# Optimization experiments

Measured on AMD Instinct MI355X. Metric: run time of the kernel, lower is better.

The kernel has to match this reference:

```python
import jax, jax.numpy as jnp
import numpy as np

EPS = 1e-5
H_PN = 64      # PointNet hidden
D = 768        # hidden_dim
SEM = 512


def _ln(x, g, b):
    m = jnp.mean(x, axis=-1, keepdims=True)
    v = jnp.var(x, axis=-1, keepdims=True)
    return (x - m) * jax.lax.rsqrt(v + EPS) * g + b


def _pointnet(x, idx, num_nodes, w1, b1, g1, be1, w2, b2, w3, b3, g2, be2, w4, b4):
    # mlp1: Linear -> LN -> ReLU -> Linear  on [P, 3] points
    h = jax.nn.relu(_ln(x @ w1 + b1, g1, be1)) @ w2 + b2          # [P, 64]
    # scatter_max into per-node features (torch_scatter fills empty segments with 0)
    xg = jax.ops.segment_max(h, idx, num_segments=num_nodes)       # [num_nodes, 64]
    xg = jnp.where(jnp.isfinite(xg), xg, 0.0)
    # mlp2: Linear -> LN -> ReLU -> Linear
    return jax.nn.relu(_ln(xg @ w3 + b3, g2, be2)) @ w4 + b4       # [num_nodes, D]


def setup_inputs() -> dict:
    key = jax.random.key(0)
    ks = jax.random.split(key, 40)
    P = 1048576
    NN = 16384
    d = {
        "x_pos": jax.random.normal(ks[0], (P, 3), jnp.float32),
        "pos_batch_idx": jax.random.randint(ks[1], (P,), 0, NN),
        "x_aff": jax.random.normal(ks[2], (P, 3), jnp.float32),
        "aff_batch_idx": jax.random.randint(ks[3], (P,), 0, NN),
        "x_sem": jax.random.normal(ks[4], (NN, SEM), jnp.float32),
        "num_nodes": NN,
    }
    def lin(k, fan_in, fan_out):
        k1, k2 = jax.random.split(k)
        return (jax.random.normal(k1, (fan_in, fan_out), jnp.float32) * 0.02,
                jax.random.normal(k2, (fan_out,), jnp.float32) * 0.02)
    i = 5
    for pfx in ("pos", "aff"):
        d[pfx + "_w1"], d[pfx + "_b1"] = lin(ks[i], 3, H_PN); i += 1
        d[pfx + "_g1"] = jnp.ones((H_PN,), jnp.float32)
        d[pfx + "_be1"] = jnp.zeros((H_PN,), jnp.float32)
        d[pfx + "_w2"], d[pfx + "_b2"] = lin(ks[i], H_PN, H_PN); i += 1
        d[pfx + "_w3"], d[pfx + "_b3"] = lin(ks[i], H_PN, D); i += 1
        d[pfx + "_g2"] = jnp.ones((D,), jnp.float32)
        d[pfx + "_be2"] = jnp.zeros((D,), jnp.float32)
        d[pfx + "_w4"], d[pfx + "_b4"] = lin(ks[i], D, D); i += 1
    d["sem_w"], d["sem_b"] = lin(ks[i], SEM, D); i += 1
    d["fus_w"], d["fus_b"] = lin(ks[i], 3 * D, D); i += 1
    d["fus_g"] = jnp.ones((D,), jnp.float32)
    d["fus_be"] = jnp.zeros((D,), jnp.float32)
    return d


def reference(x_pos, pos_batch_idx, x_aff, aff_batch_idx, x_sem, num_nodes,
              pos_w1, pos_b1, pos_g1, pos_be1, pos_w2, pos_b2, pos_w3, pos_b3,
              pos_g2, pos_be2, pos_w4, pos_b4,
              aff_w1, aff_b1, aff_g1, aff_be1, aff_w2, aff_b2, aff_w3, aff_b3,
              aff_g2, aff_be2, aff_w4, aff_b4,
              sem_w, sem_b, fus_w, fus_b, fus_g, fus_be):
    h_pos = _pointnet(x_pos, pos_batch_idx, num_nodes, pos_w1, pos_b1, pos_g1,
                      pos_be1, pos_w2, pos_b2, pos_w3, pos_b3, pos_g2, pos_be2,
                      pos_w4, pos_b4)
    h_aff = _pointnet(x_aff, aff_batch_idx, num_nodes, aff_w1, aff_b1, aff_g1,
                      aff_be1, aff_w2, aff_b2, aff_w3, aff_b3, aff_g2, aff_be2,
                      aff_w4, aff_b4)
    h_sem = x_sem @ sem_w + sem_b                                  # [NN, D]
    h = jnp.concatenate([h_pos, h_aff, h_sem], axis=-1)            # [NN, 3D]
    return jax.nn.relu(_ln(h @ fus_w + fus_b, fus_g, fus_be))      # [NN, D]
```

## Files before the change

### kernel.cpp

```cpp
#include <hip/hip_runtime.h>

typedef __attribute__((ext_vector_type(8))) __bf16 bf16x8;
typedef __attribute__((ext_vector_type(4))) float floatx4;

#define NN 16384
#define EPS 1e-5f

__device__ __forceinline__ unsigned short f2b(float f) {
  unsigned u = __float_as_uint(f);
  u += 0x7fffu + ((u >> 16) & 1u);
  return (unsigned short)(u >> 16);
}
__device__ __forceinline__ float b2f(unsigned short u) {
  return __uint_as_float(((unsigned)u) << 16);
}

__device__ __forceinline__ void gl_lds16(const void* g, void* l) {
  __builtin_amdgcn_global_load_lds(
      (const __attribute__((address_space(1))) void*)(unsigned long long)g,
      (__attribute__((address_space(3))) void*)(unsigned long long)l, 16, 0, 0);
}

__global__ void RoboNodeEncoder_88424786690347_kernel() {}

__global__ __launch_bounds__(256) void zero_u32(unsigned* __restrict__ p, int n) {
  int i = blockIdx.x * blockDim.x + threadIdx.x;
  if (i < n) p[i] = 0u;
}

__global__ __launch_bounds__(256) void convert3(const float* __restrict__ a, int na,
                                                const float* __restrict__ b, int nb,
                                                const float* __restrict__ c, int nc,
                                                unsigned short* __restrict__ out) {
  int i = blockIdx.x * 256 + threadIdx.x;
  int total = na + nb + nc;
  if (i >= total) return;
  float v;
  if (i < na) v = a[i];
  else if (i < na + nb) v = b[i - na];
  else v = c[i - na - nb];
  out[i] = f2b(v);
}

__global__ __launch_bounds__(256) void convert_sem(const float* __restrict__ in,
                                                   unsigned short* __restrict__ out) {
  int i = blockIdx.x * 256 + threadIdx.x;
  const float4* p = reinterpret_cast<const float4*>(in);
  float4 fa = p[2 * i];
  float4 fb = p[2 * i + 1];
  uint4 pk;
  pk.x = (unsigned)f2b(fa.x) | ((unsigned)f2b(fa.y) << 16);
  pk.y = (unsigned)f2b(fa.z) | ((unsigned)f2b(fa.w) << 16);
  pk.z = (unsigned)f2b(fb.x) | ((unsigned)f2b(fb.y) << 16);
  pk.w = (unsigned)f2b(fb.z) | ((unsigned)f2b(fb.w) << 16);
  reinterpret_cast<uint4*>(out)[i] = pk;
}

__global__ __launch_bounds__(256) void transpose_f32_b16(const float* __restrict__ in,
                                                         unsigned short* __restrict__ out,
                                                         int R, int C) {
  __shared__ float t[32][33];
  int bx = blockIdx.x * 32, by = blockIdx.y * 32;
  int x = threadIdx.x, y = threadIdx.y;
#pragma unroll
  for (int i = 0; i < 32; i += 8) t[y + i][x] = in[(size_t)(by + y + i) * C + bx + x];
  __syncthreads();
#pragma unroll
  for (int i = 0; i < 32; i += 8) out[(size_t)(bx + y + i) * R + by + x] = f2b(t[x][y + i]);
}

__global__ __launch_bounds__(256) void transpose_w3_pair(const float* __restrict__ pw3,
                                                         const float* __restrict__ aw3,
                                                         unsigned short* __restrict__ w3T) {
  __shared__ float t[32][33];
  const float* in = blockIdx.z ? aw3 : pw3;
  unsigned short* out = w3T + (size_t)blockIdx.z * 768 * 64;
  int R = 64, C = 768;
  int bx = blockIdx.x * 32, by = blockIdx.y * 32;
  int x = threadIdx.x, y = threadIdx.y;
#pragma unroll
  for (int i = 0; i < 32; i += 8) t[y + i][x] = in[(size_t)(by + y + i) * C + bx + x];
  __syncthreads();
#pragma unroll
  for (int i = 0; i < 32; i += 8) out[(size_t)(bx + y + i) * R + by + x] = f2b(t[x][y + i]);
}

__global__ void prep_pointnet2(const float* __restrict__ w1p, const float* __restrict__ b1p,
                               const float* __restrict__ g1p,
                               const float* __restrict__ w1a, const float* __restrict__ b1a,
                               const float* __restrict__ g1a,
                               const float* __restrict__ w2p, const float* __restrict__ w2a,
                               float* __restrict__ G2, float* __restrict__ Mq2,
                               unsigned short* __restrict__ w2T) {
  int br = blockIdx.x;
  const float* w1 = br ? w1a : w1p;
  const float* b1 = br ? b1a : b1p;
  const float* g1 = br ? g1a : g1p;
  const float* w2 = br ? w2a : w2p;
  float* G = G2 + br * 256;
  float* Mq = Mq2 + br * 16;
  unsigned short* w2t = w2T + br * 4096;
  int k = threadIdx.x;
#pragma unroll
  for (int n = 0; n < 64; n++) w2t[n * 64 + k] = f2b(w2[k * 64 + n]);
  float c[4] = {w1[k], w1[64 + k], w1[128 + k], b1[k]};
#pragma unroll
  for (int a = 0; a < 4; a++) {
    float s = c[a];
#pragma unroll
    for (int off = 32; off > 0; off >>= 1) s += __shfl_xor(s, off, 64);
    c[a] -= s * (1.f / 64.f);
  }
  float g = g1[k];
#pragma unroll
  for (int a = 0; a < 4; a++) G[a * 64 + k] = c[a] * g;
  const int AA[10] = {0, 1, 2, 3, 0, 0, 0, 1, 1, 2};
  const int BB[10] = {0, 1, 2, 3, 1, 2, 3, 2, 3, 3};
#pragma unroll
  for (int t = 0; t < 10; t++) {
    float s = c[AA[t]] * c[BB[t]];
#pragma unroll
    for (int off = 32; off > 0; off >>= 1) s += __shfl_xor(s, off, 64);
    s *= (1.f / 64.f);
    if (t >= 4) s *= 2.f;
    if (k == 0) Mq[t] = s;
  }
}

__global__ __launch_bounds__(256) void hist_bucket(const int* __restrict__ pos_idx,
                                                   const int* __restrict__ aff_idx, int P,
                                                   unsigned* __restrict__ cntB) {
  __shared__ unsigned lc[512];
  int br = blockIdx.y;
  const int* idx = br ? aff_idx : pos_idx;
  for (int i = threadIdx.x; i < 512; i += 256) lc[i] = 0u;
  __syncthreads();
  int stride = gridDim.x * blockDim.x;
  for (int i = blockIdx.x * blockDim.x + threadIdx.x; i < P; i += stride)
    atomicAdd(&lc[idx[i] >> 5], 1u);
  __syncthreads();
  for (int i = threadIdx.x; i < 512; i += 256)
    if (lc[i]) atomicAdd(&cntB[br * 512 + i], lc[i]);
}

__global__ __launch_bounds__(512) void scan_bucket(const unsigned* __restrict__ cntB,
                                                   unsigned* __restrict__ offsB,
                                                   unsigned* __restrict__ curB) {
  int br = blockIdx.x;
  __shared__ unsigned ps[512];
  int t = threadIdx.x;
  unsigned v = cntB[br * 512 + t];
  ps[t] = v;
  __syncthreads();
  for (int off = 1; off < 512; off <<= 1) {
    unsigned a = (t >= off) ? ps[t - off] : 0u;
    __syncthreads();
    ps[t] += a;
    __syncthreads();
  }
  unsigned excl = ps[t] - v;
  offsB[br * 513 + t] = excl;
  curB[br * 512 + t] = excl;
  if (t == 511) offsB[br * 513 + 512] = ps[t];
}

__global__ __launch_bounds__(256) void bucket_scatter(
    const float* __restrict__ x_pos, const float* __restrict__ x_aff,
    const int* __restrict__ pos_idx, const int* __restrict__ aff_idx, int P,
    unsigned* __restrict__ curB, float4* __restrict__ sortedB) {
  __shared__ unsigned lcnt[512], lbase[512];
  int br = blockIdx.y;
  const float* x = br ? x_aff : x_pos;
  const int* idx = br ? aff_idx : pos_idx;
  float4* sorted = sortedB + (size_t)br * P;
  int nb = gridDim.x;
  int chunk = (P + nb - 1) / nb;
  int start = blockIdx.x * chunk;
  int end = start + chunk;
  if (end > P) end = P;
  for (int i = threadIdx.x; i < 512; i += 256) lcnt[i] = 0u;
  __syncthreads();
  for (int i = start + threadIdx.x; i < end; i += 256)
    atomicAdd(&lcnt[idx[i] >> 5], 1u);
  __syncthreads();
  for (int i = threadIdx.x; i < 512; i += 256) {
    unsigned c = lcnt[i];
    lbase[i] = c ? atomicAdd(&curB[br * 512 + i], c) : 0u;
  }
  __syncthreads();
  for (int i = threadIdx.x; i < 512; i += 256) lcnt[i] = 0u;
  __syncthreads();
  for (int i = start + threadIdx.x; i < end; i += 256) {
    int nd = idx[i];
    int b = nd >> 5;
    unsigned lo = atomicAdd(&lcnt[b], 1u);
    float4 v;
    v.x = x[3 * i]; v.y = x[3 * i + 1]; v.z = x[3 * i + 2];
    v.w = __int_as_float(nd & 31);
    sorted[lbase[b] + lo] = v;
  }
}

__global__ __launch_bounds__(256) void bucket_mlp_max(
    const float4* __restrict__ sortedB, const unsigned* __restrict__ offsB,
    const float* __restrict__ G2, const float* __restrict__ Mq2,
    const float* __restrict__ be1p, const float* __restrict__ be1a,
    const unsigned short* __restrict__ w2T,
    const float* __restrict__ b2p, const float* __restrict__ b2a,
    unsigned short* __restrict__ xgB, int P) {
  __shared__ __align__(16) unsigned short hs[4][64 * 64];
  __shared__ int ndl[4][64];
  __shared__ unsigned nmaxU[32 * 64];
  int br = blockIdx.y;
  int bucket = blockIdx.x;
  const float4* sorted = sortedB + (size_t)br * P;
  const unsigned* offs = offsB + br * 513;
  const float* G = G2 + br * 256;
  const float* Mq = Mq2 + br * 16;
  const float* be1 = br ? be1a : be1p;
  const unsigned short* w2t = w2T + br * 4096;
  const float* b2 = br ? b2a : b2p;
  unsigned short* out = xgB + (size_t)br * NN * 64;

  int tid = threadIdx.x;
  int lane = tid & 63, w = tid >> 6;
  int lr = lane & 15, quad = lane >> 4;
  int l7 = lane & 7;

  for (int e = tid; e < 2048; e += 256) nmaxU[e] = 0u;

  bf16x8 bfr[4][2];
#pragma unroll
  for (int j = 0; j < 4; j++)
#pragma unroll
    for (int s = 0; s < 2; s++)
      bfr[j][s] = *reinterpret_cast<const bf16x8*>(&w2t[(j * 16 + lr) * 64 + s * 32 + quad * 8]);
  float M00 = Mq[0], M11 = Mq[1], M22 = Mq[2], M33 = Mq[3];
  float T01 = Mq[4], T02 = Mq[5], T03 = Mq[6], T12 = Mq[7], T13 = Mq[8], T23 = Mq[9];
  __syncthreads();

  int seg0 = (int)offs[bucket], seg1 = (int)offs[bucket + 1];
  unsigned short* hrow = &hs[w][0];
  for (int t0 = seg0 + w * 64; t0 < seg1; t0 += 256) {
    int pi = t0 + lane;
    if (pi >= seg1) pi = seg1 - 1;
    float4 xv = sorted[pi];
    float x0 = xv.x, x1 = xv.y, x2 = xv.z;
    ndl[w][lane] = __float_as_int(xv.w);
    float var = M33 + x0 * fmaf(M00, x0, fmaf(T01, x1, fmaf(T02, x2, T03)))
                    + x1 * fmaf(M11, x1, fmaf(T12, x2, T13))
                    + x2 * fmaf(M22, x2, T23);
    float rstd = rsqrtf(var + EPS);
    float x0r = x0 * rstd, x1r = x1 * rstd, x2r = x2 * rstd;
#pragma unroll
    for (int c = 0; c < 8; c++) {
      bf16x8 hv;
#pragma unroll
      for (int e = 0; e < 8; e++) {
        int k = c * 8 + e;
        float y = fmaf(x0r, G[k], fmaf(x1r, G[64 + k],
                  fmaf(x2r, G[128 + k], fmaf(rstd, G[192 + k], be1[k]))));
        hv[e] = (__bf16)fmaxf(y, 0.f);
      }
      *reinterpret_cast<bf16x8*>(&hrow[lane * 64 + ((c ^ l7) << 3)]) = hv;
    }
    asm volatile("s_waitcnt lgkmcnt(0)" ::: "memory");
#pragma unroll
    for (int i = 0; i < 4; i++) {
      int row = i * 16 + lr;
      bf16x8 a0 = *reinterpret_cast<const bf16x8*>(&hrow[row * 64 + ((quad ^ l7) << 3)]);
      bf16x8 a1 = *reinterpret_cast<const bf16x8*>(&hrow[row * 64 + (((4 + quad) ^ l7) << 3)]);
      floatx4 accj[4] = {};
#pragma unroll
      for (int j = 0; j < 4; j++) {
        accj[j] = __builtin_amdgcn_mfma_f32_16x16x32_bf16(a0, bfr[j][0], accj[j], 0, 0, 0);
        accj[j] = __builtin_amdgcn_mfma_f32_16x16x32_bf16(a1, bfr[j][1], accj[j], 0, 0, 0);
      }
      int nd0 = ndl[w][i * 16 + quad * 4 + 0];
      int nd1 = ndl[w][i * 16 + quad * 4 + 1];
      int nd2 = ndl[w][i * 16 + quad * 4 + 2];
      int nd3 = ndl[w][i * 16 + quad * 4 + 3];
#pragma unroll
      for (int j = 0; j < 4; j++) {
        int col = j * 16 + lr;
#pragma unroll
        for (int r = 0; r < 4; r++) {
          unsigned u = __float_as_uint(accj[j][r]);
          unsigned ord = (u & 0x80000000u) ? ~u : (u | 0x80000000u);
          int nd = (r == 0) ? nd0 : (r == 1) ? nd1 : (r == 2) ? nd2 : nd3;
          atomicMax(&nmaxU[nd * 64 + col], ord);
        }
      }
    }
  }
  __syncthreads();
  for (int e = tid; e < 2048; e += 256) {
    unsigned u = nmaxU[e];
    int f = e & 63;
    float val;
    if (u == 0u) val = 0.f;
    else {
      float m = (u & 0x80000000u) ? __uint_as_float(u ^ 0x80000000u) : __uint_as_float(~u);
      val = m + b2[f];
    }
    out[(size_t)(bucket * 32 + (e >> 6)) * 64 + f] = f2b(val);
  }
}

__device__ __forceinline__ void gemm_core(
    const unsigned short* __restrict__ A, int lda,
    const unsigned short* __restrict__ BT, int ldb,
    const float* __restrict__ bias,
    unsigned short* __restrict__ C, int ldc, int colOff, int K,
    int m0, int n0) {
  __shared__ __align__(16) unsigned short As[128 * 32];
  __shared__ __align__(16) unsigned short Bs[128 * 32];
  int tid = threadIdx.x;
  int lane = tid & 63, w = tid >> 6;
  int wm = (w >> 1) * 64, wn = (w & 1) * 64;
  int lr = lane & 15, quad = lane >> 4;
  int lgr = lane >> 2;
  int lgc = (lane & 3) << 3;
  floatx4 acc[4][4] = {};

  for (int k0 = 0; k0 < K; k0 += 32) {
    __syncthreads();
#pragma unroll
    for (int s = 0; s < 2; s++) {
      int r = w * 16 + s * 64;
      gl_lds16(&A[(size_t)(m0 + r + lgr) * lda + k0 + lgc], &As[r * 32]);
      gl_lds16(&BT[(size_t)(n0 + r + lgr) * ldb + k0 + lgc], &Bs[r * 32]);
    }
    __syncthreads();
    bf16x8 a[4], b[4];
#pragma unroll
    for (int i = 0; i < 4; i++)
      a[i] = *reinterpret_cast<const bf16x8*>(&As[(wm + i * 16 + lr) * 32 + quad * 8]);
#pragma unroll
    for (int j = 0; j < 4; j++)
      b[j] = *reinterpret_cast<const bf16x8*>(&Bs[(wn + j * 16 + lr) * 32 + quad * 8]);
#pragma unroll
    for (int i = 0; i < 4; i++)
#pragma unroll
      for (int j = 0; j < 4; j++)
        acc[i][j] = __builtin_amdgcn_mfma_f32_16x16x32_bf16(a[i], b[j], acc[i][j], 0, 0, 0);
  }
#pragma unroll
  for (int j = 0; j < 4; j++) {
    int gcol = n0 + wn + j * 16 + lr;
    float bv = bias ? bias[gcol] : 0.0f;
#pragma unroll
    for (int i = 0; i < 4; i++) {
#pragma unroll
      for (int r = 0; r < 4; r++) {
        int grow = m0 + wm + i * 16 + quad * 4 + r;
        C[(size_t)grow * ldc + colOff + gcol] = f2b(acc[i][j][r] + bv);
      }
    }
  }
}

__global__ __launch_bounds__(256) void gemm_fold(const unsigned short* __restrict__ fusT,
                                                 const unsigned short* __restrict__ wB,
                                                 unsigned short* __restrict__ BTcat) {
  int z = blockIdx.z;
  if (z == 2 && blockIdx.x >= 4) return;
  gemm_core(fusT + z * 768, 2304, wB + (size_t)z * 589824, 768, nullptr,
            BTcat, 2048, z * 768, 768, blockIdx.y * 128, blockIdx.x * 128);
}

__global__ __launch_bounds__(256) void gemm_w3(const unsigned short* __restrict__ xgB,
                                               const unsigned short* __restrict__ w3T,
                                               const float* __restrict__ pb3,
                                               const float* __restrict__ ab3,
                                               unsigned short* __restrict__ t) {
  int z = blockIdx.z;
  gemm_core(xgB + (size_t)z * NN * 64, 64, w3T + (size_t)z * 768 * 64, 64,
            z ? ab3 : pb3, t + (size_t)z * NN * 768, 768, 0, 64,
            blockIdx.y * 128, blockIdx.x * 128);
}

template <int SEMBF>
__global__ __launch_bounds__(256) void gemm_fuse3_v2(
    const unsigned short* __restrict__ A0, const unsigned short* __restrict__ A1,
    const unsigned short* __restrict__ A2b, const float* __restrict__ A2f,
    const unsigned short* __restrict__ BT,
    const float* __restrict__ bias, unsigned short* __restrict__ C) {
  __shared__ __align__(16) unsigned short As[128 * 32];
  __shared__ __align__(16) unsigned short Bs[128 * 32];
  int tid = threadIdx.x;
  int lid = blockIdx.x;
  int sg = lid / 48, rem = lid % 48;
  int n_t = rem >> 3;
  int m_t = sg * 8 + (rem & 7);
  int m0 = m_t * 128, n0 = n_t * 128;
  int lane = tid & 63, w = tid >> 6;
  int wm = (w >> 1) * 64, wn = (w & 1) * 64;
  int lr = lane & 15, quad = lane >> 4;
  int lgr = lane >> 2;
  int lgc = (lane & 3) << 3;
  floatx4 acc[4][4] = {};

  for (int k0 = 0; k0 < 2048; k0 += 32) {
    __syncthreads();
#pragma unroll
    for (int s = 0; s < 2; s++) {
      int r = w * 16 + s * 64;
      gl_lds16(&BT[(size_t)(n0 + r + lgr) * 2048 + k0 + lgc], &Bs[r * 32]);
    }
    if (!SEMBF && k0 >= 1536) {
      int kk = k0 - 1536;
#pragma unroll
      for (int s = 0; s < 2; s++) {
        int cc = tid + s * 256;
        int row = cc >> 2, kc = (cc & 3) << 3;
        const float* src = &A2f[(size_t)(m0 + row) * 512 + kk + kc];
        float4 fa = *reinterpret_cast<const float4*>(src);
        float4 fb = *reinterpret_cast<const float4*>(src + 4);
        uint4 pk;
        pk.x = (unsigned)f2b(fa.x) | ((unsigned)f2b(fa.y) << 16);
        pk.y = (unsigned)f2b(fa.z) | ((unsigned)f2b(fa.w) << 16);
        pk.z = (unsigned)f2b(fb.x) | ((unsigned)f2b(fb.y) << 16);
        pk.w = (unsigned)f2b(fb.z) | ((unsigned)f2b(fb.w) << 16);
        *reinterpret_cast<uint4*>(&As[row * 32 + kc]) = pk;
      }
    } else {
      const unsigned short* Ap;
      int kk, ldA;
      if (k0 < 768) { Ap = A0; kk = k0; ldA = 768; }
      else if (k0 < 1536) { Ap = A1; kk = k0 - 768; ldA = 768; }
      else { Ap = A2b; kk = k0 - 1536; ldA = 512; }
#pragma unroll
      for (int s = 0; s < 2; s++) {
        int r = w * 16 + s * 64;
        gl_lds16(&Ap[(size_t)(m0 + r + lgr) * ldA + kk + lgc], &As[r * 32]);
      }
    }
    __syncthreads();
    bf16x8 a[4], b[4];
#pragma unroll
    for (int i = 0; i < 4; i++)
      a[i] = *reinterpret_cast<const bf16x8*>(&As[(wm + i * 16 + lr) * 32 + quad * 8]);
#pragma unroll
    for (int j = 0; j < 4; j++)
      b[j] = *reinterpret_cast<const bf16x8*>(&Bs[(wn + j * 16 + lr) * 32 + quad * 8]);
#pragma unroll
    for (int i = 0; i < 4; i++)
#pragma unroll
      for (int j = 0; j < 4; j++)
        acc[i][j] = __builtin_amdgcn_mfma_f32_16x16x32_bf16(a[i], b[j], acc[i][j], 0, 0, 0);
  }
#pragma unroll
  for (int j = 0; j < 4; j++) {
    int gcol = n0 + wn + j * 16 + lr;
    float bv = bias[gcol];
#pragma unroll
    for (int i = 0; i < 4; i++) {
#pragma unroll
      for (int r = 0; r < 4; r++) {
        int grow = m0 + wm + i * 16 + quad * 4 + r;
        C[(size_t)grow * 768 + gcol] = f2b(acc[i][j][r] + bv);
      }
    }
  }
}

__global__ __launch_bounds__(256) void fuse_bias(
    const float* __restrict__ fus_b, const float* __restrict__ fus_w,
    const float* __restrict__ pb4, const float* __restrict__ ab4,
    const float* __restrict__ semb, float* __restrict__ bias_tot) {
  int c = blockIdx.x;
  int tid = threadIdx.x;
  float s = 0.f;
  for (int j = tid; j < 768; j += 256) {
    s = fmaf(pb4[j],  fus_w[(size_t)j * 768 + c], s);
    s = fmaf(ab4[j],  fus_w[(size_t)(768 + j) * 768 + c], s);
    s = fmaf(semb[j], fus_w[(size_t)(1536 + j) * 768 + c], s);
  }
#pragma unroll
  for (int off = 32; off > 0; off >>= 1) s += __shfl_xor(s, off, 64);
  __shared__ float sm[4];
  if ((tid & 63) == 0) sm[tid >> 6] = s;
  __syncthreads();
  if (tid == 0) bias_tot[c] = sm[0] + sm[1] + sm[2] + sm[3] + fus_b[c];
}

__global__ __launch_bounds__(256) void ln2(unsigned short* __restrict__ tB,
                                           const float* __restrict__ pg2,
                                           const float* __restrict__ pbe2,
                                           const float* __restrict__ ag2,
                                           const float* __restrict__ abe2) {
  int br = blockIdx.y;
  unsigned short* X = tB + (size_t)br * NN * 768;
  const float* g = br ? ag2 : pg2;
  const float* be = br ? abe2 : pbe2;
  int row = blockIdx.x, tid = threadIdx.x;
  size_t base = (size_t)row * 768;
  float xv[3];
#pragma unroll
  for (int i = 0; i < 3; i++) xv[i] = b2f(X[base + tid + i * 256]);
  float s = xv[0] + xv[1] + xv[2];
  float q = xv[0] * xv[0] + xv[1] * xv[1] + xv[2] * xv[2];
#pragma unroll
  for (int off = 32; off > 0; off >>= 1) {
    s += __shfl_xor(s, off, 64);
    q += __shfl_xor(q, off, 64);
  }
  __shared__ float ss[4], qq[4];
  int w = tid >> 6, lane = tid & 63;
  if (lane == 0) { ss[w] = s; qq[w] = q; }
  __syncthreads();
  s = ss[0] + ss[1] + ss[2] + ss[3];
  q = qq[0] + qq[1] + qq[2] + qq[3];
  float m = s * (1.0f / 768.0f);
  float v = fmaf(-m, m, q * (1.0f / 768.0f));
  float rstd = rsqrtf(v + EPS);
#pragma unroll
  for (int i = 0; i < 3; i++) {
    int c = tid + i * 256;
    float y = (xv[i] - m) * rstd * g[c] + be[c];
    X[base + c] = f2b(fmaxf(y, 0.0f));
  }
}

__global__ __launch_bounds__(256) void ln_relu_768_f32(
    const unsigned short* __restrict__ X, const float* __restrict__ g,
    const float* __restrict__ be, float* __restrict__ Y) {
  int row = blockIdx.x, tid = threadIdx.x;
  size_t base = (size_t)row * 768;
  float xv[3];
#pragma unroll
  for (int i = 0; i < 3; i++) xv[i] = b2f(X[base + tid + i * 256]);
  float s = xv[0] + xv[1] + xv[2];
  float q = xv[0] * xv[0] + xv[1] * xv[1] + xv[2] * xv[2];
#pragma unroll
  for (int off = 32; off > 0; off >>= 1) {
    s += __shfl_xor(s, off, 64);
    q += __shfl_xor(q, off, 64);
  }
  __shared__ float ss[4], qq[4];
  int w = tid >> 6, lane = tid & 63;
  if (lane == 0) { ss[w] = s; qq[w] = q; }
  __syncthreads();
  s = ss[0] + ss[1] + ss[2] + ss[3];
  q = qq[0] + qq[1] + qq[2] + qq[3];
  float m = s * (1.0f / 768.0f);
  float v = fmaf(-m, m, q * (1.0f / 768.0f));
  float rstd = rsqrtf(v + EPS);
#pragma unroll
  for (int i = 0; i < 3; i++) {
    int c = tid + i * 256;
    float y = (xv[i] - m) * rstd * g[c] + be[c];
    Y[base + c] = fmaxf(y, 0.0f);
  }
}

extern "C" void kernel_launch(void* const* d_in, const int* in_sizes, int n_in,
                              void* d_out, int out_size, void* d_ws, size_t ws_size,
                              hipStream_t stream) {
  typedef const float* cf;
  cf x_pos = (cf)d_in[0];
  const int* pos_idx = (const int*)d_in[1];
  cf x_aff = (cf)d_in[2];
  const int* aff_idx = (const int*)d_in[3];
  cf x_sem = (cf)d_in[4];
  cf pw1 = (cf)d_in[6],  pb1 = (cf)d_in[7],  pg1 = (cf)d_in[8],  pbe1 = (cf)d_in[9];
  cf pw2 = (cf)d_in[10], pb2 = (cf)d_in[11];
  cf pw3 = (cf)d_in[12], pb3 = (cf)d_in[13], pg2 = (cf)d_in[14], pbe2 = (cf)d_in[15];
  cf pw4 = (cf)d_in[16], pb4 = (cf)d_in[17];
  cf aw1 = (cf)d_in[18], ab1 = (cf)d_in[19], ag1 = (cf)d_in[20], abe1 = (cf)d_in[21];
  cf aw2 = (cf)d_in[22], ab2 = (cf)d_in[23];
  cf aw3 = (cf)d_in[24], ab3 = (cf)d_in[25], ag2 = (cf)d_in[26], abe2 = (cf)d_in[27];
  cf aw4 = (cf)d_in[28], ab4 = (cf)d_in[29];
  cf semw = (cf)d_in[30], semb = (cf)d_in[31];
  cf fusw = (cf)d_in[32], fusb = (cf)d_in[33], fusg = (cf)d_in[34], fusbe = (cf)d_in[35];

  int P = in_sizes[0] / 3;

  char* wsb = (char*)d_ws;
  size_t off = 0;
  auto carve = [&](size_t bytes) -> void* {
    void* p = wsb + off;
    off = (off + bytes + 255) & ~(size_t)255;
    return p;
  };
  unsigned short* xgB   = (unsigned short*)carve((size_t)2 * NN * 64 * 2);
  unsigned short* t     = (unsigned short*)carve((size_t)2 * NN * 768 * 2);
  float4* sorted        = (float4*)carve((size_t)2 * P * 16);
  unsigned short* F = (unsigned short*)sorted;
  unsigned short* w3T   = (unsigned short*)carve((size_t)2 * 768 * 64 * 2);
  unsigned short* fusT  = (unsigned short*)carve((size_t)768 * 2304 * 2);
  unsigned short* wB    = (unsigned short*)carve((size_t)1572864 * 2);
  unsigned short* BTcat = (unsigned short*)carve((size_t)768 * 2048 * 2);
  unsigned short* w2T   = (unsigned short*)carve((size_t)2 * 4096 * 2);
  float* bias_tot = (float*)carve((size_t)768 * 4);
  float* G2  = (float*)carve((size_t)512 * 4);
  float* Mq2 = (float*)carve((size_t)32 * 4);
  unsigned* bcnt  = (unsigned*)carve((size_t)2 * 512 * 4);
  unsigned* boffs = (unsigned*)carve((size_t)2 * 513 * 4);
  unsigned* bcur  = (unsigned*)carve((size_t)2 * 512 * 4);
  unsigned short* semB = (unsigned short*)carve((size_t)NN * 512 * 2);
  bool sem_bf = (off <= ws_size);

  zero_u32<<<(1024 + 255) / 256, 256, 0, stream>>>(bcnt, 1024);

  dim3 tb(32, 8);
  transpose_w3_pair<<<dim3(24, 2, 2), tb, 0, stream>>>(pw3, aw3, w3T);
  transpose_f32_b16<<<dim3(24, 72), tb, 0, stream>>>(fusw, fusT, 2304, 768);
  convert3<<<(1572864 + 255) / 256, 256, 0, stream>>>(pw4, 589824, aw4, 589824,
                                                      semw, 393216, wB);
  if (sem_bf)
    convert_sem<<<(NN * 512 / 8) / 256, 256, 0, stream>>>(x_sem, semB);
  prep_pointnet2<<<2, 64, 0, stream>>>(pw1, pb1, pg1, aw1, ab1, ag1, pw2, aw2,
                                       G2, Mq2, w2T);

  gemm_fold<<<dim3(6, 6, 3), 256, 0, stream>>>(fusT, wB, BTcat);
  fuse_bias<<<768, 256, 0, stream>>>(fusb, fusw, pb4, ab4, semb, bias_tot);

  hist_bucket<<<dim3(64, 2), 256, 0, stream>>>(pos_idx, aff_idx, P, bcnt);
  scan_bucket<<<2, 512, 0, stream>>>(bcnt, boffs, bcur);
  bucket_scatter<<<dim3(256, 2), 256, 0, stream>>>(x_pos, x_aff, pos_idx, aff_idx,
                                                   P, bcur, sorted);
  bucket_mlp_max<<<dim3(512, 2), 256, 0, stream>>>(sorted, boffs, G2, Mq2, pbe1, abe1,
                                                   w2T, pb2, ab2, xgB, P);

  gemm_w3<<<dim3(6, NN / 128, 2), 256, 0, stream>>>(xgB, w3T, pb3, ab3, t);
  ln2<<<dim3(NN, 2), 256, 0, stream>>>(t, pg2, pbe2, ag2, abe2);

  if (sem_bf)
    gemm_fuse3_v2<1><<<768, 256, 0, stream>>>(t, t + (size_t)NN * 768, semB, x_sem,
                                              BTcat, bias_tot, F);
  else
    gemm_fuse3_v2<0><<<768, 256, 0, stream>>>(t, t + (size_t)NN * 768, nullptr, x_sem,
                                              BTcat, bias_tot, F);
  ln_relu_768_f32<<<NN, 256, 0, stream>>>(F, fusg, fusbe, (float*)d_out);
}
```

Measured before the change: 502.7 us.

## Fuse W3 GEMM with LayerNorm+ReLU and store sorted points as fp16

Replaces the separate gemm_w3 and ln2 kernels with one kernel. It computes a 32-row by 768-column tile per block with MFMA, reduces the row statistics across the four waves through LDS, and writes the normalized, ReLU'd bf16 output directly. This removes one full write-then-read round trip of the 2x16384x768 bf16 intermediate. Separately, the bucket-sorted point records shrink from float4 to ushort4, with coordinates in fp16, which halves the scatter write and the MLP read traffic at the cost of input precision.

```diff
diff --git a/kernel.cpp b/kernel.cpp
--- a/kernel.cpp
+++ b/kernel.cpp
@@ -1,4 +1,5 @@
 #include <hip/hip_runtime.h>
+#include <hip/hip_fp16.h>
 
 typedef __attribute__((ext_vector_type(8))) __bf16 bf16x8;
 typedef __attribute__((ext_vector_type(4))) float floatx4;
@@ -167,12 +168,12 @@
 __global__ __launch_bounds__(256) void bucket_scatter(
     const float* __restrict__ x_pos, const float* __restrict__ x_aff,
     const int* __restrict__ pos_idx, const int* __restrict__ aff_idx, int P,
-    unsigned* __restrict__ curB, float4* __restrict__ sortedB) {
+    unsigned* __restrict__ curB, ushort4* __restrict__ sortedB) {
   __shared__ unsigned lcnt[512], lbase[512];
   int br = blockIdx.y;
   const float* x = br ? x_aff : x_pos;
   const int* idx = br ? aff_idx : pos_idx;
-  float4* sorted = sortedB + (size_t)br * P;
+  ushort4* sorted = sortedB + (size_t)br * P;
   int nb = gridDim.x;
   int chunk = (P + nb - 1) / nb;
   int start = blockIdx.x * chunk;
@@ -194,15 +195,17 @@
     int nd = idx[i];
     int b = nd >> 5;
     unsigned lo = atomicAdd(&lcnt[b], 1u);
-    float4 v;
-    v.x = x[3 * i]; v.y = x[3 * i + 1]; v.z = x[3 * i + 2];
-    v.w = __int_as_float(nd & 31);
+    ushort4 v;
+    v.x = __half_as_ushort(__float2half(x[3 * i]));
+    v.y = __half_as_ushort(__float2half(x[3 * i + 1]));
+    v.z = __half_as_ushort(__float2half(x[3 * i + 2]));
+    v.w = (unsigned short)(nd & 31);
     sorted[lbase[b] + lo] = v;
   }
 }
 
 __global__ __launch_bounds__(256) void bucket_mlp_max(
-    const float4* __restrict__ sortedB, const unsigned* __restrict__ offsB,
+    const ushort4* __restrict__ sortedB, const unsigned* __restrict__ offsB,
     const float* __restrict__ G2, const float* __restrict__ Mq2,
     const float* __restrict__ be1p, const float* __restrict__ be1a,
     const unsigned short* __restrict__ w2T,
@@ -213,7 +216,7 @@
   __shared__ unsigned nmaxU[32 * 64];
   int br = blockIdx.y;
   int bucket = blockIdx.x;
-  const float4* sorted = sortedB + (size_t)br * P;
+  const ushort4* sorted = sortedB + (size_t)br * P;
   const unsigned* offs = offsB + br * 513;
   const float* G = G2 + br * 256;
   const float* Mq = Mq2 + br * 16;
@@ -244,9 +247,11 @@
   for (int t0 = seg0 + w * 64; t0 < seg1; t0 += 256) {
     int pi = t0 + lane;
     if (pi >= seg1) pi = seg1 - 1;
-    float4 xv = sorted[pi];
-    float x0 = xv.x, x1 = xv.y, x2 = xv.z;
-    ndl[w][lane] = __float_as_int(xv.w);
+    ushort4 xv = sorted[pi];
+    float x0 = __half2float(__ushort_as_half(xv.x));
+    float x1 = __half2float(__ushort_as_half(xv.y));
+    float x2 = __half2float(__ushort_as_half(xv.z));
+    ndl[w][lane] = (int)xv.w;
     float var = M33 + x0 * fmaf(M00, x0, fmaf(T01, x1, fmaf(T02, x2, T03)))
                     + x1 * fmaf(M11, x1, fmaf(T12, x2, T13))
                     + x2 * fmaf(M22, x2, T23);
@@ -369,15 +374,113 @@
             BTcat, 2048, z * 768, 768, blockIdx.y * 128, blockIdx.x * 128);
 }
 
-__global__ __launch_bounds__(256) void gemm_w3(const unsigned short* __restrict__ xgB,
-                                               const unsigned short* __restrict__ w3T,
-                                               const float* __restrict__ pb3,
-                                               const float* __restrict__ ab3,
-                                               unsigned short* __restrict__ t) {
-  int z = blockIdx.z;
-  gemm_core(xgB + (size_t)z * NN * 64, 64, w3T + (size_t)z * 768 * 64, 64,
-            z ? ab3 : pb3, t + (size_t)z * NN * 768, 768, 0, 64,
-            blockIdx.y * 128, blockIdx.x * 128);
+__global__ __launch_bounds__(256) void gemm_w3_ln(
+    const unsigned short* __restrict__ xgB, const unsigned short* __restrict__ w3T,
+    const float* __restrict__ pb3, const float* __restrict__ ab3,
+    const float* __restrict__ pg2, const float* __restrict__ pbe2,
+    const float* __restrict__ ag2, const float* __restrict__ abe2,
+    unsigned short* __restrict__ tB) {
+  __shared__ __align__(16) unsigned short As[32 * 64];
+  __shared__ float pstat[4][32][2];
+  int br = blockIdx.y;
+  const unsigned short* A = xgB + (size_t)br * NN * 64;
+  const unsigned short* BT = w3T + (size_t)br * 768 * 64;
+  const float* b3 = br ? ab3 : pb3;
+  const float* g  = br ? ag2 : pg2;
+  const float* be = br ? abe2 : pbe2;
+  unsigned short* out = tB + (size_t)br * NN * 768;
+  int m0 = blockIdx.x * 32;
+  int tid = threadIdx.x;
+  int lane = tid & 63, w = tid >> 6;
+  int lr = lane & 15, quad = lane >> 4;
+
+  gl_lds16(&A[(size_t)(m0 + (tid >> 3)) * 64 + (tid & 7) * 8], &As[(w << 6) * 8]);
+  __syncthreads();
+
+  bf16x8 a[2][2];
+#pragma unroll
+  for (int i = 0; i < 2; i++)
+#pragma unroll
+    for (int s = 0; s < 2; s++)
+      a[i][s] = *reinterpret_cast<const bf16x8*>(&As[(i * 16 + lr) * 64 + s * 32 + quad * 8]);
+
+  int c0 = w * 192;
+  float b3v[12];
+#pragma unroll
+  for (int nt = 0; nt < 12; nt++) b3v[nt] = b3[c0 + nt * 16 + lr];
+
+  floatx4 acc[2][12] = {};
+#pragma unroll
+  for (int nt = 0; nt < 12; nt++) {
+    int col = c0 + nt * 16 + lr;
+    bf16x8 b0 = *reinterpret_cast<const bf16x8*>(&BT[(size_t)col * 64 + quad * 8]);
+    bf16x8 b1 = *reinterpret_cast<const bf16x8*>(&BT[(size_t)col * 64 + 32 + quad * 8]);
+#pragma unroll
+    for (int i = 0; i < 2; i++) {
+      acc[i][nt] = __builtin_amdgcn_mfma_f32_16x16x32_bf16(a[i][0], b0, acc[i][nt], 0, 0, 0);
+      acc[i][nt] = __builtin_amdgcn_mfma_f32_16x16x32_bf16(a[i][1], b1, acc[i][nt], 0, 0, 0);
+    }
+  }
+
+  float sr[2][4] = {{0.f, 0.f, 0.f, 0.f}, {0.f, 0.f, 0.f, 0.f}};
+  float qr[2][4] = {{0.f, 0.f, 0.f, 0.f}, {0.f, 0.f, 0.f, 0.f}};
+#pragma unroll
+  for (int i = 0; i < 2; i++)
+#pragma unroll
+    for (int nt = 0; nt < 12; nt++)
+#pragma unroll
+      for (int r = 0; r < 4; r++) {
+        float v = acc[i][nt][r] + b3v[nt];
+        acc[i][nt][r] = v;
+        sr[i][r] += v;
+        qr[i][r] = fmaf(v, v, qr[i][r]);
+      }
+#pragma unroll
+  for (int off = 1; off < 16; off <<= 1) {
+#pragma unroll
+    for (int i = 0; i < 2; i++)
+#pragma unroll
+      for (int r = 0; r < 4; r++) {
+        sr[i][r] += __shfl_xor(sr[i][r], off, 64);
+        qr[i][r] += __shfl_xor(qr[i][r], off, 64);
+      }
+  }
+  if (lr == 0) {
+#pragma unroll
+    for (int i = 0; i < 2; i++)
+#pragma unroll
+      for (int r = 0; r < 4; r++) {
+        pstat[w][i * 16 + quad * 4 + r][0] = sr[i][r];
+        pstat[w][i * 16 + quad * 4 + r][1] = qr[i][r];
+      }
+  }
+  __syncthreads();
+  float mrow[2][4], rrow[2][4];
+#pragma unroll
+  for (int i = 0; i < 2; i++)
+#pragma unroll
+    for (int r = 0; r < 4; r++) {
+      int row = i * 16 + quad * 4 + r;
+      float S = pstat[0][row][0] + pstat[1][row][0] + pstat[2][row][0] + pstat[3][row][0];
+      float Q = pstat[0][row][1] + pstat[1][row][1] + pstat[2][row][1] + pstat[3][row][1];
+      float mm = S * (1.0f / 768.0f);
+      float vv = fmaf(-mm, mm, Q * (1.0f / 768.0f));
+      mrow[i][r] = mm;
+      rrow[i][r] = rsqrtf(vv + EPS);
+    }
+#pragma unroll
+  for (int nt = 0; nt < 12; nt++) {
+    int col = c0 + nt * 16 + lr;
+    float gv = g[col], bev = be[col];
+#pragma unroll
+    for (int i = 0; i < 2; i++)
+#pragma unroll
+      for (int r = 0; r < 4; r++) {
+        int row = m0 + i * 16 + quad * 4 + r;
+        float y = (acc[i][nt][r] - mrow[i][r]) * rrow[i][r] * gv + bev;
+        out[(size_t)row * 768 + col] = f2b(fmaxf(y, 0.0f));
+      }
+  }
 }
 
 template <int SEMBF>
@@ -485,44 +588,6 @@
   if (tid == 0) bias_tot[c] = sm[0] + sm[1] + sm[2] + sm[3] + fus_b[c];
 }
 
-__global__ __launch_bounds__(256) void ln2(unsigned short* __restrict__ tB,
-                                           const float* __restrict__ pg2,
-                                           const float* __restrict__ pbe2,
-                                           const float* __restrict__ ag2,
-                                           const float* __restrict__ abe2) {
-  int br = blockIdx.y;
-  unsigned short* X = tB + (size_t)br * NN * 768;
-  const float* g = br ? ag2 : pg2;
-  const float* be = br ? abe2 : pbe2;
-  int row = blockIdx.x, tid = threadIdx.x;
-  size_t base = (size_t)row * 768;
-  float xv[3];
-#pragma unroll
-  for (int i = 0; i < 3; i++) xv[i] = b2f(X[base + tid + i * 256]);
-  float s = xv[0] + xv[1] + xv[2];
-  float q = xv[0] * xv[0] + xv[1] * xv[1] + xv[2] * xv[2];
-#pragma unroll
-  for (int off = 32; off > 0; off >>= 1) {
-    s += __shfl_xor(s, off, 64);
-    q += __shfl_xor(q, off, 64);
-  }
-  __shared__ float ss[4], qq[4];
-  int w = tid >> 6, lane = tid & 63;
-  if (lane == 0) { ss[w] = s; qq[w] = q; }
-  __syncthreads();
-  s = ss[0] + ss[1] + ss[2] + ss[3];
-  q = qq[0] + qq[1] + qq[2] + qq[3];
-  float m = s * (1.0f / 768.0f);
-  float v = fmaf(-m, m, q * (1.0f / 768.0f));
-  float rstd = rsqrtf(v + EPS);
-#pragma unroll
-  for (int i = 0; i < 3; i++) {
-    int c = tid + i * 256;
-    float y = (xv[i] - m) * rstd * g[c] + be[c];
-    X[base + c] = f2b(fmaxf(y, 0.0f));
-  }
-}
-
 __global__ __launch_bounds__(256) void ln_relu_768_f32(
     const unsigned short* __restrict__ X, const float* __restrict__ g,
     const float* __restrict__ be, float* __restrict__ Y) {
@@ -586,7 +651,7 @@
   };
   unsigned short* xgB   = (unsigned short*)carve((size_t)2 * NN * 64 * 2);
   unsigned short* t     = (unsigned short*)carve((size_t)2 * NN * 768 * 2);
-  float4* sorted        = (float4*)carve((size_t)2 * P * 16);
+  ushort4* sorted       = (ushort4*)carve((size_t)2 * P * 16);
   unsigned short* F = (unsigned short*)sorted;
   unsigned short* w3T   = (unsigned short*)carve((size_t)2 * 768 * 64 * 2);
   unsigned short* fusT  = (unsigned short*)carve((size_t)768 * 2304 * 2);
@@ -624,8 +689,8 @@
   bucket_mlp_max<<<dim3(512, 2), 256, 0, stream>>>(sorted, boffs, G2, Mq2, pbe1, abe1,
                                                    w2T, pb2, ab2, xgB, P);
 
-  gemm_w3<<<dim3(6, NN / 128, 2), 256, 0, stream>>>(xgB, w3T, pb3, ab3, t);
-  ln2<<<dim3(NN, 2), 256, 0, stream>>>(t, pg2, pbe2, ag2, abe2);
+  gemm_w3_ln<<<dim3(NN / 32, 2), 256, 0, stream>>>(xgB, w3T, pb3, ab3,
+                                                   pg2, pbe2, ag2, abe2, t);
 
   if (sem_bf)
     gemm_fuse3_v2<1><<<768, 256, 0, stream>>>(t, t + (size_t)NN * 768, semB, x_sem,
```

Measured after the change: 482.3 us. 4.1% less time.
